# Performance work log

Measured on AMD Instinct MI355X. Metric: run time of the kernel, lower is better.

The kernel has to match this reference:

```python
import jax, jax.numpy as jnp
import numpy as np

N_QUBITS = 4
N_QLAYERS = 2
B = 524288


def setup_inputs() -> dict:
    key = jax.random.key(0)
    ks = jax.random.split(key, 12)
    s = 0.1
    return {
        "x": jax.random.normal(ks[0], (B, 2), jnp.float32),
        "enc_w1": jax.random.normal(ks[1], (2, 64), jnp.float32) * s,
        "enc_b1": jnp.zeros((64,), jnp.float32),
        "enc_w2": jax.random.normal(ks[2], (64, 16), jnp.float32) * s,
        "enc_b2": jnp.zeros((16,), jnp.float32),
        "pre_w": jax.random.normal(ks[3], (16, N_QUBITS), jnp.float32) * s,
        "pre_b": jnp.zeros((N_QUBITS,), jnp.float32),
        "q_weights": jax.random.uniform(ks[4], (N_QLAYERS, N_QUBITS), jnp.float32, 0.0, 2.0 * np.pi),
        "post_w1": jax.random.normal(ks[5], (N_QUBITS, 32), jnp.float32) * s,
        "post_b1": jnp.zeros((32,), jnp.float32),
        "post_w2": jax.random.normal(ks[6], (32, 4), jnp.float32) * s,
        "post_b2": jnp.zeros((4,), jnp.float32),
    }


def _ry(state, theta, q):
    # state: [B,2,2,2,2] real statevector; theta: scalar or [B]
    c, sn = jnp.cos(theta / 2), jnp.sin(theta / 2)
    if jnp.ndim(c) == 1:  # per-sample angle (embedding)
        c = c[:, None, None, None]
        sn = sn[:, None, None, None]
    st = jnp.moveaxis(state, q + 1, -1)
    new = jnp.stack([c * st[..., 0] - sn * st[..., 1],
                     sn * st[..., 0] + c * st[..., 1]], axis=-1)
    return jnp.moveaxis(new, -1, q + 1)


def _cnot(state, ctrl, tgt):
    st = jnp.moveaxis(state, (ctrl + 1, tgt + 1), (-2, -1))
    st = jnp.concatenate([st[..., 0:1, :], st[..., 1:2, ::-1]], axis=-2)
    return jnp.moveaxis(st, (-2, -1), (ctrl + 1, tgt + 1))


def q_layer(q_in, q_weights):
    # batched 4-qubit circuit: RY embedding + BasicEntanglerLayers, <Z_i> readout
    b = q_in.shape[0]
    state = jnp.zeros((b, 2 ** N_QUBITS), q_in.dtype).at[:, 0].set(1.0)
    state = state.reshape((b,) + (2,) * N_QUBITS)
    for q in range(N_QUBITS):
        state = _ry(state, q_in[:, q], q)
    for l in range(N_QLAYERS):
        for q in range(N_QUBITS):
            state = _ry(state, q_weights[l, q], q)
        for c_, t_ in [(0, 1), (1, 2), (2, 3), (3, 0)]:
            state = _cnot(state, c_, t_)
    probs = state * state  # real amplitudes -> probabilities
    exps = []
    for q in range(N_QUBITS):
        axes = tuple(a for a in range(1, N_QUBITS + 1) if a != q + 1)
        marg = probs.sum(axes)  # [B,2]
        exps.append(marg[:, 0] - marg[:, 1])
    return jnp.stack(exps, axis=-1)  # [B,4]


def reference(x, enc_w1, enc_b1, enc_w2, enc_b2, pre_w, pre_b, q_weights,
              post_w1, post_b1, post_w2, post_b2):
    z = jnp.tanh(x @ enc_w1 + enc_b1)
    z = jnp.tanh(z @ enc_w2 + enc_b2)
    q_in = z @ pre_w + pre_b
    q_out = q_layer(q_in, q_weights)
    h = jnp.tanh(q_out @ post_w1 + post_b1)
    return h @ post_w2 + post_b2
```

## Files before the change

### kernel.cpp

```cpp
#include <hip/hip_runtime.h>
#include <math.h>

#define NQ 4
#define NL 2

typedef _Float16 f16;
typedef _Float16 f16x8 __attribute__((ext_vector_type(8)));
typedef float f32x4 __attribute__((ext_vector_type(4)));

#define K_TANH 2.885390081777927f
#define BETA   0.07957747154594767f

__device__ __forceinline__ float tanh4(float a) {
    float e = __builtin_amdgcn_exp2f(a);
    float r = __builtin_amdgcn_rcpf(e + 1.0f);
    return fmaf(-2.0f, r, 1.0f);
}
__device__ __forceinline__ float tanh5(float a) {
    return tanh4(a * K_TANH);
}

__device__ __forceinline__ void sincos_rev(float t, float* s, float* c) {
    float f = __builtin_amdgcn_fractf(t);
    *s = __builtin_amdgcn_sinf(f);
    *c = __builtin_amdgcn_cosf(f);
}

__shared__ float z2s[256][20];
__shared__ float qtrig[16];

extern "C" __global__ void __launch_bounds__(256)
hybrid_pinn_kernel(const float* __restrict__ x,
                   const float* __restrict__ ew1, const float* __restrict__ eb1,
                   const float* __restrict__ ew2, const float* __restrict__ eb2,
                   const float* __restrict__ pw,  const float* __restrict__ pb,
                   const float* __restrict__ qw,
                   const float* __restrict__ pw1, const float* __restrict__ pb1,
                   const float* __restrict__ pw2, const float* __restrict__ pb2,
                   float* __restrict__ out)
{
    const int tid   = threadIdx.x;
    const int lane  = tid & 63;
    const int wbase = (tid >> 6) * 64;
    const int brow0 = blockIdx.x * 256;
    const int ak    = (lane >> 4) * 8;
    const int bn    = lane & 15;

    if (tid < 8) {
        float s, c;
        __sincosf(0.5f * qw[tid], &s, &c);
        qtrig[tid] = c; qtrig[8 + tid] = s;
    }
    __syncthreads();

    f16x8 bfrag0, bfrag1;
#pragma unroll
    for (int j = 0; j < 8; ++j) {
        bfrag0[j] = (f16)(ew2[(ak + j) * 16 + bn] * K_TANH);
        bfrag1[j] = (f16)(ew2[(32 + ak + j) * 16 + bn] * K_TANH);
    }

    const float2* x2 = reinterpret_cast<const float2*>(x);
    float2 xr[4];
#pragma unroll
    for (int mt = 0; mt < 4; ++mt)
        xr[mt] = x2[brow0 + wbase + (lane & 15) + mt * 16];

    f16x8 afrag[4][2];
#pragma unroll
    for (int kt = 0; kt < 2; ++kt) {
        const int base = kt * 32 + ak;
        float w0[8], w1[8], bb[8];
        *reinterpret_cast<float4*>(&w0[0]) = *reinterpret_cast<const float4*>(&ew1[base]);
        *reinterpret_cast<float4*>(&w0[4]) = *reinterpret_cast<const float4*>(&ew1[base + 4]);
        *reinterpret_cast<float4*>(&w1[0]) = *reinterpret_cast<const float4*>(&ew1[64 + base]);
        *reinterpret_cast<float4*>(&w1[4]) = *reinterpret_cast<const float4*>(&ew1[64 + base + 4]);
        *reinterpret_cast<float4*>(&bb[0]) = *reinterpret_cast<const float4*>(&eb1[base]);
        *reinterpret_cast<float4*>(&bb[4]) = *reinterpret_cast<const float4*>(&eb1[base + 4]);
#pragma unroll
        for (int j = 0; j < 8; ++j) {
            w0[j] *= K_TANH; w1[j] *= K_TANH; bb[j] *= K_TANH;
        }
#pragma unroll
        for (int mt = 0; mt < 4; ++mt) {
#pragma unroll
            for (int j = 0; j < 8; ++j) {
                float a = fmaf(xr[mt].y, w1[j], fmaf(xr[mt].x, w0[j], bb[j]));
                afrag[mt][kt][j] = (f16)tanh4(a);
            }
        }
    }

    const float ebc = eb2[bn] * K_TANH;
    f32x4 acc[4];
#pragma unroll
    for (int mt = 0; mt < 4; ++mt) {
        f32x4 z = {ebc, ebc, ebc, ebc};
        z = __builtin_amdgcn_mfma_f32_16x16x32_f16(afrag[mt][0], bfrag0, z, 0, 0, 0);
        z = __builtin_amdgcn_mfma_f32_16x16x32_f16(afrag[mt][1], bfrag1, z, 0, 0, 0);
        acc[mt] = z;
    }
#pragma unroll
    for (int mt = 0; mt < 4; ++mt) {
#pragma unroll
        for (int j = 0; j < 4; ++j)
            z2s[wbase + mt * 16 + (lane >> 4) * 4 + j][bn] = acc[mt][j];
    }

    float z2[16];
    {
        float4 r0 = *reinterpret_cast<const float4*>(&z2s[tid][0]);
        float4 r1 = *reinterpret_cast<const float4*>(&z2s[tid][4]);
        float4 r2 = *reinterpret_cast<const float4*>(&z2s[tid][8]);
        float4 r3 = *reinterpret_cast<const float4*>(&z2s[tid][12]);
        z2[0]=r0.x; z2[1]=r0.y; z2[2]=r0.z; z2[3]=r0.w;
        z2[4]=r1.x; z2[5]=r1.y; z2[6]=r1.z; z2[7]=r1.w;
        z2[8]=r2.x; z2[9]=r2.y; z2[10]=r2.z; z2[11]=r2.w;
        z2[12]=r3.x; z2[13]=r3.y; z2[14]=r3.z; z2[15]=r3.w;
    }
#pragma unroll
    for (int j = 0; j < 16; ++j) z2[j] = tanh4(z2[j]);

    float tq[NQ];
#pragma unroll
    for (int j = 0; j < NQ; ++j) tq[j] = pb[j];
#pragma unroll
    for (int i = 0; i < 16; ++i) {
        float zi = z2[i];
#pragma unroll
        for (int j = 0; j < NQ; ++j)
            tq[j] = fmaf(zi, pw[i * NQ + j], tq[j]);
    }
#pragma unroll
    for (int j = 0; j < NQ; ++j) tq[j] *= BETA;

    float cq[NQ], sq[NQ];
#pragma unroll
    for (int q = 0; q < NQ; ++q)
        sincos_rev(tq[q], &sq[q], &cq[q]);

    float ab[4], cd[4];
#pragma unroll
    for (int h = 0; h < 4; ++h) {
        ab[h] = ((h & 2) ? sq[0] : cq[0]) * ((h & 1) ? sq[1] : cq[1]);
        cd[h] = ((h & 2) ? sq[2] : cq[2]) * ((h & 1) ? sq[3] : cq[3]);
    }
    float st[16];
#pragma unroll
    for (int i = 0; i < 16; ++i)
        st[i] = ab[i >> 2] * cd[i & 3];

#pragma unroll
    for (int l = 0; l < NL; ++l) {
#pragma unroll
        for (int q = 0; q < NQ; ++q) {
            const float cc = qtrig[l * NQ + q];
            const float ss = qtrig[8 + l * NQ + q];
            const int bit = 8 >> q;
#pragma unroll
            for (int i = 0; i < 16; ++i) {
                if (i & bit) continue;
                float a0 = st[i], a1 = st[i | bit];
                st[i]       = fmaf(cc, a0, -ss * a1);
                st[i | bit] = fmaf(ss, a0,  cc * a1);
            }
        }
        const int cn[4][2] = {{8, 4}, {4, 2}, {2, 1}, {1, 8}};
#pragma unroll
        for (int k = 0; k < 4; ++k) {
            const int bc = cn[k][0], bt = cn[k][1];
#pragma unroll
            for (int i = 0; i < 16; ++i) {
                if ((i & bc) && !(i & bt)) {
                    float t = st[i];
                    st[i] = st[i | bt];
                    st[i | bt] = t;
                }
            }
        }
    }

    float p[16];
#pragma unroll
    for (int i = 0; i < 16; ++i) p[i] = st[i] * st[i];

    float e[8], d[8];
#pragma unroll
    for (int i = 0; i < 8; ++i) { e[i] = p[2*i] + p[2*i+1]; d[i] = p[2*i] - p[2*i+1]; }
    float f0 = e[0] + e[1], f1 = e[2] + e[3], f2 = e[4] + e[5], f3 = e[6] + e[7];
    float qo[NQ];
    qo[3] = ((d[0]+d[1]) + (d[2]+d[3])) + ((d[4]+d[5]) + (d[6]+d[7]));
    qo[2] = ((e[0]-e[1]) + (e[2]-e[3])) + ((e[4]-e[5]) + (e[6]-e[7]));
    qo[1] = (f0 - f1) + (f2 - f3);
    qo[0] = (f0 + f1) - (f2 + f3);

    float h[32];
#pragma unroll
    for (int j = 0; j < 32; ++j) {
        float a = pb1[j];
#pragma unroll
        for (int i = 0; i < NQ; ++i)
            a = fmaf(qo[i], pw1[i * 32 + j], a);
        h[j] = tanh5(a);
    }

    float o[4];
#pragma unroll
    for (int j = 0; j < 4; ++j) o[j] = pb2[j];
#pragma unroll
    for (int i = 0; i < 32; ++i) {
        float hi = h[i];
#pragma unroll
        for (int j = 0; j < 4; ++j)
            o[j] = fmaf(hi, pw2[i * 4 + j], o[j]);
    }

    reinterpret_cast<float4*>(out)[brow0 + tid] = make_float4(o[0], o[1], o[2], o[3]);
}

extern "C" void kernel_launch(void* const* d_in, const int* in_sizes, int n_in,
                              void* d_out, int out_size, void* d_ws, size_t ws_size,
                              hipStream_t stream) {
    const float* x   = (const float*)d_in[0];
    const float* ew1 = (const float*)d_in[1];
    const float* eb1 = (const float*)d_in[2];
    const float* ew2 = (const float*)d_in[3];
    const float* eb2 = (const float*)d_in[4];
    const float* pw  = (const float*)d_in[5];
    const float* pb  = (const float*)d_in[6];
    const float* qw  = (const float*)d_in[7];
    const float* pw1 = (const float*)d_in[8];
    const float* pb1 = (const float*)d_in[9];
    const float* pw2 = (const float*)d_in[10];
    const float* pb2 = (const float*)d_in[11];
    float* out = (float*)d_out;

    const int rows = in_sizes[0] / 2;
    hipLaunchKernelGGL(hybrid_pinn_kernel, dim3(rows / 256), dim3(256), 0, stream,
                       x, ew1, eb1, ew2, eb2, pw, pb, qw,
                       pw1, pb1, pw2, pb2, out);
}
```

Before: 29.52 us.

## Replace statevector simulation with closed-form expectation polynomials

The per-thread 16-amplitude statevector simulation is replaced by closed-form trigonometric expressions for the four Z expectations. The first-layer weight rotations are folded into the embedding angles, so double angles are used directly. Second-layer cos/sin products are precomputed per block in shared memory. The shared staging array is also padded to 17 columns and read with scalar loads instead of float4. This removes most per-thread FMAs and register pressure, but it relies on the hand-derived algebra being exact for this circuit and changes floating-point rounding.

```diff
diff --git a/kernel.cpp b/kernel.cpp
--- a/kernel.cpp
+++ b/kernel.cpp
@@ -2,14 +2,13 @@
 #include <math.h>
 
 #define NQ 4
-#define NL 2
 
 typedef _Float16 f16;
 typedef _Float16 f16x8 __attribute__((ext_vector_type(8)));
 typedef float f32x4 __attribute__((ext_vector_type(4)));
 
 #define K_TANH 2.885390081777927f
-#define BETA   0.07957747154594767f
+#define BETA2  0.15915494309189535f
 
 __device__ __forceinline__ float tanh4(float a) {
     float e = __builtin_amdgcn_exp2f(a);
@@ -20,14 +19,8 @@
     return tanh4(a * K_TANH);
 }
 
-__device__ __forceinline__ void sincos_rev(float t, float* s, float* c) {
-    float f = __builtin_amdgcn_fractf(t);
-    *s = __builtin_amdgcn_sinf(f);
-    *c = __builtin_amdgcn_cosf(f);
-}
-
-__shared__ float z2s[256][20];
-__shared__ float qtrig[16];
+__shared__ float z2s[256][17];
+__shared__ float cpre[12];
 
 extern "C" __global__ void __launch_bounds__(256)
 hybrid_pinn_kernel(const float* __restrict__ x,
@@ -46,10 +39,11 @@
     const int ak    = (lane >> 4) * 8;
     const int bn    = lane & 15;
 
-    if (tid < 8) {
+    if (tid < 4) {
         float s, c;
-        __sincosf(0.5f * qw[tid], &s, &c);
-        qtrig[tid] = c; qtrig[8 + tid] = s;
+        __sincosf(qw[4 + tid], &s, &c);
+        cpre[tid] = c; cpre[4 + tid] = s;
+        cpre[8 + tid] = qw[tid] * BETA2;
     }
     __syncthreads();
 
@@ -108,16 +102,8 @@
     }
 
     float z2[16];
-    {
-        float4 r0 = *reinterpret_cast<const float4*>(&z2s[tid][0]);
-        float4 r1 = *reinterpret_cast<const float4*>(&z2s[tid][4]);
-        float4 r2 = *reinterpret_cast<const float4*>(&z2s[tid][8]);
-        float4 r3 = *reinterpret_cast<const float4*>(&z2s[tid][12]);
-        z2[0]=r0.x; z2[1]=r0.y; z2[2]=r0.z; z2[3]=r0.w;
-        z2[4]=r1.x; z2[5]=r1.y; z2[6]=r1.z; z2[7]=r1.w;
-        z2[8]=r2.x; z2[9]=r2.y; z2[10]=r2.z; z2[11]=r2.w;
-        z2[12]=r3.x; z2[13]=r3.y; z2[14]=r3.z; z2[15]=r3.w;
-    }
+#pragma unroll
+    for (int j = 0; j < 16; ++j) z2[j] = z2s[tid][j];
 #pragma unroll
     for (int j = 0; j < 16; ++j) z2[j] = tanh4(z2[j]);
 
@@ -131,68 +117,41 @@
         for (int j = 0; j < NQ; ++j)
             tq[j] = fmaf(zi, pw[i * NQ + j], tq[j]);
     }
-#pragma unroll
-    for (int j = 0; j < NQ; ++j) tq[j] *= BETA;
-
-    float cq[NQ], sq[NQ];
-#pragma unroll
-    for (int q = 0; q < NQ; ++q)
-        sincos_rev(tq[q], &sq[q], &cq[q]);
-
-    float ab[4], cd[4];
-#pragma unroll
-    for (int h = 0; h < 4; ++h) {
-        ab[h] = ((h & 2) ? sq[0] : cq[0]) * ((h & 1) ? sq[1] : cq[1]);
-        cd[h] = ((h & 2) ? sq[2] : cq[2]) * ((h & 1) ? sq[3] : cq[3]);
-    }
-    float st[16];
-#pragma unroll
-    for (int i = 0; i < 16; ++i)
-        st[i] = ab[i >> 2] * cd[i & 3];
-
-#pragma unroll
-    for (int l = 0; l < NL; ++l) {
-#pragma unroll
-        for (int q = 0; q < NQ; ++q) {
-            const float cc = qtrig[l * NQ + q];
-            const float ss = qtrig[8 + l * NQ + q];
-            const int bit = 8 >> q;
-#pragma unroll
-            for (int i = 0; i < 16; ++i) {
-                if (i & bit) continue;
-                float a0 = st[i], a1 = st[i | bit];
-                st[i]       = fmaf(cc, a0, -ss * a1);
-                st[i | bit] = fmaf(ss, a0,  cc * a1);
-            }
-        }
-        const int cn[4][2] = {{8, 4}, {4, 2}, {2, 1}, {1, 8}};
-#pragma unroll
-        for (int k = 0; k < 4; ++k) {
-            const int bc = cn[k][0], bt = cn[k][1];
-#pragma unroll
-            for (int i = 0; i < 16; ++i) {
-                if ((i & bc) && !(i & bt)) {
-                    float t = st[i];
-                    st[i] = st[i | bt];
-                    st[i | bt] = t;
-                }
-            }
-        }
-    }
-
-    float p[16];
-#pragma unroll
-    for (int i = 0; i < 16; ++i) p[i] = st[i] * st[i];
-
-    float e[8], d[8];
-#pragma unroll
-    for (int i = 0; i < 8; ++i) { e[i] = p[2*i] + p[2*i+1]; d[i] = p[2*i] - p[2*i+1]; }
-    float f0 = e[0] + e[1], f1 = e[2] + e[3], f2 = e[4] + e[5], f3 = e[6] + e[7];
+
+    float C0, C1, C2, C3, S0, S1, S2, S3;
+    {
+        float t0 = __builtin_amdgcn_fractf(fmaf(tq[0], BETA2, cpre[8]));
+        float t1 = __builtin_amdgcn_fractf(fmaf(tq[1], BETA2, cpre[9]));
+        float t2 = __builtin_amdgcn_fractf(fmaf(tq[2], BETA2, cpre[10]));
+        float t3 = __builtin_amdgcn_fractf(fmaf(tq[3], BETA2, cpre[11]));
+        S0 = __builtin_amdgcn_sinf(t0); C0 = __builtin_amdgcn_cosf(t0);
+        S1 = __builtin_amdgcn_sinf(t1); C1 = __builtin_amdgcn_cosf(t1);
+        S2 = __builtin_amdgcn_sinf(t2); C2 = __builtin_amdgcn_cosf(t2);
+        S3 = __builtin_amdgcn_sinf(t3); C3 = __builtin_amdgcn_cosf(t3);
+    }
+
+    const float c0 = cpre[0], c1 = cpre[1], c2 = cpre[2], c3 = cpre[3];
+    const float s0 = cpre[4], s1 = cpre[5], s2 = cpre[6], s3 = cpre[7];
+    const float c12 = c1 * c2, s12 = s1 * s2, sc12 = s1 * c2, cs12 = c1 * s2;
+    const float A1 = c12 * c3,  A2 = c12 * s3,  A3 = sc12 * c3, A4 = s12 * s3;
+    const float B1 = c0 * c1,   B2 = s0 * s1;
+    const float D1 = c0 * c12,  D2 = c0 * sc12, D3 = s0 * c12,  D4 = s0 * s12;
+    const float c0s12 = c0 * s12, s0s12 = s0 * s12;
+    const float E1 = D1 * c3,          E2 = (c0 * cs12) * c3;
+    const float E3 = c0s12 * c3,       E4 = D3 * s3;
+    const float E5 = (s0 * sc12) * c3, E6 = c0s12 * s3;
+    const float E7 = (s0 * cs12) * s3, E8 = s0s12 * s3;
+
+    const float C01 = C0 * C1, C13 = C1 * C3, C02 = C0 * C2, C23 = C2 * C3;
+    const float S01 = S0 * S1, S02 = S0 * S2, S12 = S1 * S2, S13 = S1 * S3;
+    const float S23 = S2 * S3, C2S3 = C2 * S3;
+
     float qo[NQ];
-    qo[3] = ((d[0]+d[1]) + (d[2]+d[3])) + ((d[4]+d[5]) + (d[6]+d[7]));
-    qo[2] = ((e[0]-e[1]) + (e[2]-e[3])) + ((e[4]-e[5]) + (e[6]-e[7]));
-    qo[1] = (f0 - f1) + (f2 - f3);
-    qo[0] = (f0 + f1) - (f2 + f3);
+    qo[0] = A1 * (C0 * C13) - A2 * (S01 * C2S3) - A3 * (S12 * C3) - A4 * S0;
+    qo[1] = B1 * (C02 * C3) + B2 * S02;
+    qo[2] = D1 * C13 - D2 * ((C0 * S12) * C3) - D3 * (S01 * C2) - D4 * (S0 * S3);
+    qo[3] = E1 * C02 - E2 * (C1 * S23) + E3 * (C0 * S13) + E4 * C2S3
+          + E5 * (S02 * C3) - E6 * ((S0 * C1) * C23) - E7 * (C01 * S2) + E8 * S1;
 
     float h[32];
 #pragma unroll
```

Result: faster. 27.33 us (-7.4%).
